# Kernel tuning notes

Measured on AMD Instinct MI355X. Metric: run time of the kernel, lower is better.

Reference implementation:

```python
import jax, jax.numpy as jnp
import numpy as np

B, S, D = 2, 1024, 2048      # batch, seq_len, hidden
H, HD = 16, 128              # heads, head_dim
FF = 8192                    # SwiGLU intermediate
R = 3                        # num_recursion
NEG = -1e9                   # additive mask fill (finfo.min analogue)
TEMP, ALPHA = 1.0, 1.0


def _rmsnorm(x, w, eps=1e-6):
    return x * jax.lax.rsqrt(jnp.mean(x * x, axis=-1, keepdims=True) + eps) * w


def _rot_half(x):
    x1, x2 = jnp.split(x, 2, axis=-1)
    return jnp.concatenate([-x2, x1], axis=-1)


def _block(x, cos, sin, sel, ln1, ln2, Wq, Wk, Wv, Wo, Wg, Wu, Wd):
    # Llama decoder layer restricted to selected tokens.
    # The torch code gathers selected tokens + their rows/cols of the 4D causal
    # mask + their RoPE embeddings, runs dense attention on the packed subset,
    # then scatters back. That is mathematically identical to dense attention
    # over the full sequence where keys are masked to selected tokens and only
    # selected-query outputs are kept (RoPE uses ORIGINAL positions in both).
    b, s, d = x.shape
    h = _rmsnorm(x, ln1)
    q = (h @ Wq).reshape(b, s, H, HD)
    k = (h @ Wk).reshape(b, s, H, HD)
    v = (h @ Wv).reshape(b, s, H, HD)
    cs = cos[None, :, None, :]
    sn = sin[None, :, None, :]
    q = q * cs + _rot_half(q) * sn
    k = k * cs + _rot_half(k) * sn
    scores = jnp.einsum('bqhd,bkhd->bhqk', q, k) / np.float32(np.sqrt(HD))
    causal = jnp.tril(jnp.ones((s, s), dtype=bool))
    allowed = causal[None, None, :, :] & sel[:, None, None, :]  # key must be selected
    attn = jax.nn.softmax(jnp.where(allowed, scores, NEG), axis=-1)
    o = jnp.einsum('bhqk,bkhd->bqhd', attn, v).reshape(b, s, d) @ Wo
    x = x + o
    h2 = _rmsnorm(x, ln2)
    return x + (jax.nn.silu(h2 @ Wg) * (h2 @ Wu)) @ Wd


def setup_inputs() -> dict:
    key = jax.random.key(0)
    ks = jax.random.split(key, 9)
    x = jax.random.normal(ks[0], (B, S, D), dtype=jnp.float32)
    # RoPE tables at original positions (what position_embeddings carries)
    inv_freq = 1.0 / (10000.0 ** (np.arange(0, HD, 2, dtype=np.float32) / HD))
    freqs = np.outer(np.arange(S, dtype=np.float32), inv_freq)
    emb = np.concatenate([freqs, freqs], axis=-1)
    cos = jnp.asarray(np.cos(emb), dtype=jnp.float32)
    sin = jnp.asarray(np.sin(emb), dtype=jnp.float32)
    sc = 0.02
    p = lambda k, shp: jax.random.normal(k, shp, dtype=jnp.float32) * sc
    return dict(
        x=x, cos=cos, sin=sin,
        w_router=p(ks[1], (D, R)),
        ln1=jnp.ones((D,), dtype=jnp.float32),
        ln2=jnp.ones((D,), dtype=jnp.float32),
        Wq=p(ks[2], (D, D)), Wk=p(ks[3], (D, D)),
        Wv=p(ks[4], (D, D)), Wo=p(ks[5], (D, D)),
        Wg=p(ks[6], (D, FF)), Wu=p(ks[7], (D, FF)), Wd=p(ks[8], (FF, D)),
    )


def reference(x, cos, sin, w_router, ln1, ln2, Wq, Wk, Wv, Wo, Wg, Wu, Wd):
    # token-level MoR routing: top-1 depth per token, token at depth r is
    # processed by blocks 0..r and its (weighted) output at depth r is final.
    probs = jax.nn.softmax((x / TEMP) @ w_router, axis=-1) * ALPHA  # [B,S,R]
    top_idx = jnp.argmax(probs, axis=-1)                            # [B,S]
    w = jnp.take_along_axis(probs, top_idx[..., None], axis=-1)     # [B,S,1]
    final_x = x
    cur = x
    for index in range(R):
        sel = top_idx >= index                                      # tokens still active
        out = _block(cur, cos, sin, sel, ln1, ln2, Wq, Wk, Wv, Wo, Wg, Wu, Wd)
        fin = (top_idx == index)[..., None]
        final_x = jnp.where(fin, out * w, final_x)                  # finished: scatter weighted
        cur = jnp.where(sel[..., None], out, cur)                   # continuing: update state
    return final_x
```

## Files before the change

### kernel.cpp

```cpp
#include <hip/hip_runtime.h>
#include <hip/hip_bf16.h>

#define B_  2
#define S_  1024
#define D_  2048
#define H_  16
#define HD_ 128
#define FF_ 8192
#define R_  3
#define T_  (B_*S_)

typedef __attribute__((ext_vector_type(8))) short bf16x8;
typedef __attribute__((ext_vector_type(4))) float f32x4;
using bf16 = __hip_bfloat16;

__device__ __forceinline__ float bf2f(short s) {
    return __uint_as_float(((unsigned)(unsigned short)s) << 16);
}
__device__ __forceinline__ unsigned f2bf_bits(float f) {
    bf16 h = __float2bfloat16(f);
    unsigned short u; __builtin_memcpy(&u, &h, 2);
    return (unsigned)u;
}
__device__ __forceinline__ unsigned pack2(float a, float b) {
    return f2bf_bits(a) | (f2bf_bits(b) << 16);
}
__device__ __forceinline__ float wsum(float v) {
    #pragma unroll
    for (int m = 32; m; m >>= 1) v += __shfl_xor(v, m);
    return v;
}
__device__ __forceinline__ void load_lds16(const void* g, void* l) {
    __builtin_amdgcn_global_load_lds((const __attribute__((address_space(1))) void*)g,
                                     (__attribute__((address_space(3))) void*)l, 16, 0, 0);
}

__global__ __launch_bounds__(256)
void transpose_cast(const float* __restrict__ W, bf16* __restrict__ Wt, int K, int N) {
    __shared__ float tile[32][33];
    const int n0 = blockIdx.x * 32, k0 = blockIdx.y * 32;
    const int c = threadIdx.x & 31, r8 = threadIdx.x >> 5;
    #pragma unroll
    for (int i = 0; i < 4; i++) {
        int r = r8 + i * 8;
        tile[r][c] = W[(long)(k0 + r) * N + n0 + c];
    }
    __syncthreads();
    #pragma unroll
    for (int i = 0; i < 4; i++) {
        int r = r8 + i * 8;
        Wt[(long)(n0 + r) * K + k0 + c] = __float2bfloat16(tile[c][r]);
    }
}

__global__ __launch_bounds__(256)
void router_k(const float* __restrict__ X, const float* __restrict__ Wr,
              int* __restrict__ top, float* __restrict__ wsel) {
    const int t = blockIdx.x * 4 + (threadIdx.x >> 6);
    const int lane = threadIdx.x & 63;
    const float* x = X + (long)t * D_;
    float a0 = 0.f, a1 = 0.f, a2 = 0.f;
    for (int j = lane; j < D_; j += 64) {
        float xv = x[j];
        a0 += xv * Wr[j * 3 + 0];
        a1 += xv * Wr[j * 3 + 1];
        a2 += xv * Wr[j * 3 + 2];
    }
    a0 = wsum(a0); a1 = wsum(a1); a2 = wsum(a2);
    if (lane == 0) {
        int arg = 0; float bm = a0;
        if (a1 > bm) { bm = a1; arg = 1; }
        if (a2 > bm) { bm = a2; arg = 2; }
        float s = expf(a0 - bm) + expf(a1 - bm) + expf(a2 - bm);
        top[t]  = arg;
        wsel[t] = 1.0f / s;
    }
}

__global__ __launch_bounds__(256)
void rmsnorm_k(const float* __restrict__ X, const float* __restrict__ G, bf16* __restrict__ Hb) {
    const int t = blockIdx.x, tid = threadIdx.x;
    const float4* xr = (const float4*)(X + (long)t * D_);
    float4 v0 = xr[tid], v1 = xr[tid + 256];
    float ss = v0.x*v0.x + v0.y*v0.y + v0.z*v0.z + v0.w*v0.w
             + v1.x*v1.x + v1.y*v1.y + v1.z*v1.z + v1.w*v1.w;
    ss = wsum(ss);
    __shared__ float red[4];
    if ((tid & 63) == 0) red[tid >> 6] = ss;
    __syncthreads();
    const float r = rsqrtf((red[0] + red[1] + red[2] + red[3]) * (1.0f / D_) + 1e-6f);
    const float4* gr = (const float4*)G;
    float4 g0 = gr[tid], g1 = gr[tid + 256];
    uint2* ob = (uint2*)(Hb + (long)t * D_);
    uint2 o;
    o.x = pack2(v0.x * r * g0.x, v0.y * r * g0.y);
    o.y = pack2(v0.z * r * g0.z, v0.w * r * g0.w);
    ob[tid] = o;
    o.x = pack2(v1.x * r * g1.x, v1.y * r * g1.y);
    o.y = pack2(v1.z * r * g1.z, v1.w * r * g1.w);
    ob[tid + 256] = o;
}

__global__ __launch_bounds__(256)
void rope_k(bf16* __restrict__ q, bf16* __restrict__ k,
            const float* __restrict__ cosb, const float* __restrict__ sinb) {
    const int idx = blockIdx.x * 256 + threadIdx.x;
    const int d = idx & 63;
    const int h = (idx >> 6) & (H_ - 1);
    const int t = idx >> 10;
    const int s = t & (S_ - 1);
    const long base = (long)t * D_ + h * HD_;
    const float c1 = cosb[s * HD_ + d],      s1 = sinb[s * HD_ + d];
    const float c2 = cosb[s * HD_ + d + 64], s2 = sinb[s * HD_ + d + 64];
    float q1 = __bfloat162float(q[base + d]), q2 = __bfloat162float(q[base + d + 64]);
    q[base + d]      = __float2bfloat16(q1 * c1 - q2 * s1);
    q[base + d + 64] = __float2bfloat16(q2 * c2 + q1 * s2);
    float k1 = __bfloat162float(k[base + d]), k2 = __bfloat162float(k[base + d + 64]);
    k[base + d]      = __float2bfloat16(k1 * c1 - k2 * s1);
    k[base + d + 64] = __float2bfloat16(k2 * c2 + k1 * s2);
}

__global__ __launch_bounds__(256)
void attn_k(const bf16* __restrict__ qb, const bf16* __restrict__ kb, const bf16* __restrict__ vb,
            const int* __restrict__ top, int rec, bf16* __restrict__ aob) {
    __shared__ bf16 Ks[64 * 128];
    __shared__ unsigned Vt[128 * 32];
    __shared__ unsigned short Pt[4][64 * 16];
    const int tid = threadIdx.x, w = tid >> 6, lane = tid & 63;
    const int l15 = lane & 15, lg = lane >> 4;
    const int q0 = blockIdx.x * 64;
    const int h = blockIdx.y, b = blockIdx.z;
    const int qw = q0 + w * 16;

    bf16x8 Qf[4];
    {
        const bf16* qptr = qb + ((long)((b * S_ + qw + l15) * H_ + h)) * HD_ + lg * 8;
        #pragma unroll
        for (int ds = 0; ds < 4; ds++) Qf[ds] = *(const bf16x8*)(qptr + ds * 32);
    }

    f32x4 oacc[8] = {};
    float mrow[4] = {-1e30f, -1e30f, -1e30f, -1e30f};
    float lrow[4] = {0.f, 0.f, 0.f, 0.f};
    const float rs = 0.088388347648318447f;
    const int bsrc = (l15 >> 2) << 4;
    const int jj = l15 & 3;

    const int nch = blockIdx.x + 1;
    for (int kc = 0; kc < nch; kc++) {
        __syncthreads();
        #pragma unroll
        for (int i = 0; i < 4; i++) {
            int r = w * 16 + i * 4 + lg;
            int key = kc * 64 + r;
            const bf16* src = kb + ((long)((b * S_ + key) * H_ + h)) * HD_ + ((l15 ^ (r & 7)) * 8);
            load_lds16(src, &Ks[(w * 16 + i * 4) * 128]);
        }
        #pragma unroll
        for (int i = 0; i < 2; i++) {
            int j = i * 256 + tid;
            int c = j & 15, r2 = (j >> 4) & 31;
            long gv = ((long)((b * S_ + kc * 64 + 2 * r2) * H_ + h)) * HD_ + c * 8;
            uint4 va = *(const uint4*)&vb[gv];
            uint4 vbn = *(const uint4*)&vb[gv + D_];
            const unsigned short* pa = (const unsigned short*)&va;
            const unsigned short* pb = (const unsigned short*)&vbn;
            #pragma unroll
            for (int e = 0; e < 8; e++) {
                int d = c * 8 + e;
                int sw = (d ^ (d >> 3)) & 7;
                Vt[d * 32 + (((r2 >> 2) ^ sw) << 2) + (r2 & 3)] =
                    (unsigned)pa[e] | ((unsigned)pb[e] << 16);
            }
        }
        __syncthreads();

        f32x4 sacc[4] = {};
        #pragma unroll
        for (int kg = 0; kg < 4; kg++) {
            const int row = kg * 16 + l15;
            #pragma unroll
            for (int ds = 0; ds < 4; ds++) {
                bf16x8 kf = *(const bf16x8*)&Ks[row * 128 + (((ds * 4 + lg) ^ (row & 7)) * 8)];
                sacc[kg] = __builtin_amdgcn_mfma_f32_16x16x32_bf16(Qf[ds], kf, sacc[kg], 0, 0, 0);
            }
        }

        int selm[4];
        #pragma unroll
        for (int kg = 0; kg < 4; kg++) {
            int key = kc * 64 + kg * 16 + l15;
            selm[kg] = (top[b * S_ + key] >= rec) ? (key) : (1 << 30);
        }
        float pmat[4][4];
        #pragma unroll
        for (int kg = 0; kg < 4; kg++) {
            #pragma unroll
            for (int j = 0; j < 4; j++) {
                float s = sacc[kg][j] * rs;
                pmat[kg][j] = (selm[kg] <= qw + lg * 4 + j) ? s : -1e9f;
            }
        }
        float scj[4];
        #pragma unroll
        for (int j = 0; j < 4; j++) {
            float tm = fmaxf(fmaxf(pmat[0][j], pmat[1][j]), fmaxf(pmat[2][j], pmat[3][j]));
            #pragma unroll
            for (int m = 1; m < 16; m <<= 1) tm = fmaxf(tm, __shfl_xor(tm, m));
            float mnew = fmaxf(mrow[j], tm);
            scj[j] = __expf(mrow[j] - mnew);
            mrow[j] = mnew;
            float ps = 0.f;
            #pragma unroll
            for (int kg = 0; kg < 4; kg++) {
                float p = __expf(pmat[kg][j] - mnew);
                pmat[kg][j] = p;
                ps += p;
            }
            #pragma unroll
            for (int m = 1; m < 16; m <<= 1) ps += __shfl_xor(ps, m);
            lrow[j] = lrow[j] * scj[j] + ps;
        }
        #pragma unroll
        for (int kg = 0; kg < 4; kg++) {
            uint2 u;
            u.x = pack2(pmat[kg][0], pmat[kg][1]);
            u.y = pack2(pmat[kg][2], pmat[kg][3]);
            *(uint2*)&Pt[w][(kg * 16 + l15) * 16 + lg * 4] = u;
        }
        {
            float t0 = __shfl(scj[0], bsrc), t1 = __shfl(scj[1], bsrc);
            float t2 = __shfl(scj[2], bsrc), t3 = __shfl(scj[3], bsrc);
            float scq = (jj == 0) ? t0 : (jj == 1) ? t1 : (jj == 2) ? t2 : t3;
            #pragma unroll
            for (int dg = 0; dg < 8; dg++) {
                oacc[dg][0] *= scq; oacc[dg][1] *= scq;
                oacc[dg][2] *= scq; oacc[dg][3] *= scq;
            }
        }
        #pragma unroll
        for (int ks = 0; ks < 2; ks++) {
            bf16x8 pf;
            #pragma unroll
            for (int e = 0; e < 8; e++)
                pf[e] = (short)Pt[w][(ks * 32 + lg * 8 + e) * 16 + l15];
            #pragma unroll
            for (int dg = 0; dg < 8; dg++) {
                int d = dg * 16 + l15;
                int sw = (d ^ (d >> 3)) & 7;
                bf16x8 vf = *(const bf16x8*)&Vt[d * 32 + (((ks * 4 + lg) ^ sw) << 2)];
                oacc[dg] = __builtin_amdgcn_mfma_f32_16x16x32_bf16(vf, pf, oacc[dg], 0, 0, 0);
            }
        }
    }
    float u0 = __shfl(lrow[0], bsrc), u1 = __shfl(lrow[1], bsrc);
    float u2 = __shfl(lrow[2], bsrc), u3 = __shfl(lrow[3], bsrc);
    float lq = (jj == 0) ? u0 : (jj == 1) ? u1 : (jj == 2) ? u2 : u3;
    float li = 1.0f / lq;
    const long obase = ((long)((b * S_ + qw + l15) * H_ + h)) * HD_ + lg * 4;
    #pragma unroll
    for (int dg = 0; dg < 8; dg++) {
        #pragma unroll
        for (int jp = 0; jp < 2; jp++) {
            unsigned o = pack2(oacc[dg][jp * 2] * li, oacc[dg][jp * 2 + 1] * li);
            *(unsigned*)&aob[obase + dg * 16 + jp * 2] = o;
        }
    }
}

template<int EP>
__global__ __launch_bounds__(256)
void gemm_k(const bf16* __restrict__ A,
            const bf16* __restrict__ Bt0, const bf16* __restrict__ Bt1, const bf16* __restrict__ Bt2,
            bf16* __restrict__ C0, bf16* __restrict__ C1, bf16* __restrict__ C2,
            const float* __restrict__ resid, float* __restrict__ xout,
            int N, int K) {
    __shared__ bf16 As[128 * 32];
    __shared__ bf16 Bs[128 * 32];
    const int tid = threadIdx.x;
    const int w = tid >> 6, lane = tid & 63;

    const int gx = gridDim.x;
    const int nwg = gx * gridDim.y;
    const int orig = blockIdx.y * gx + blockIdx.x;
    const int qc = nwg >> 3, rc = nwg & 7;
    const int xcd = orig & 7, loc = orig >> 3;
    const int wg = (xcd < rc ? xcd * (qc + 1) : rc * (qc + 1) + (xcd - rc) * qc) + loc;
    const int m0 = (wg % gx) * 128, n0 = (wg / gx) * 128;

    const bf16* Bt = (blockIdx.z == 0) ? Bt0 : ((blockIdx.z == 1) ? Bt1 : Bt2);
    bf16* Cb       = (blockIdx.z == 0) ? C0  : ((blockIdx.z == 1) ? C1  : C2);

    const int srow = lane >> 2;
    const int scol = (lane & 3) * 8;
    const long gA = (long)(m0 + w * 32 + srow) * K + scol;
    const long gB = (long)(n0 + w * 32 + srow) * K + scol;

    const int wr = w >> 1, wc = w & 1;
    const int fm = lane & 15, kg = lane >> 4;

    f32x4 acc[4][4] = {};

    for (int kt = 0; kt < K; kt += 32) {
        __syncthreads();
        #pragma unroll
        for (int i = 0; i < 2; i++) {
            load_lds16(A  + gA + (long)(16 * i) * K + kt, &As[(w * 32 + 16 * i) * 32]);
            load_lds16(Bt + gB + (long)(16 * i) * K + kt, &Bs[(w * 32 + 16 * i) * 32]);
        }
        __syncthreads();
        bf16x8 af[4], bfr[4];
        #pragma unroll
        for (int mi = 0; mi < 4; mi++)
            af[mi] = *(const bf16x8*)&As[(wr * 64 + mi * 16 + fm) * 32 + kg * 8];
        #pragma unroll
        for (int ni = 0; ni < 4; ni++)
            bfr[ni] = *(const bf16x8*)&Bs[(wc * 64 + ni * 16 + fm) * 32 + kg * 8];
        #pragma unroll
        for (int mi = 0; mi < 4; mi++)
            #pragma unroll
            for (int ni = 0; ni < 4; ni++)
                acc[mi][ni] = __builtin_amdgcn_mfma_f32_16x16x32_bf16(af[mi], bfr[ni], acc[mi][ni], 0, 0, 0);
    }
    #pragma unroll
    for (int mi = 0; mi < 4; mi++) {
        #pragma unroll
        for (int j = 0; j < 4; j++) {
            const int m = m0 + wr * 64 + mi * 16 + kg * 4 + j;
            #pragma unroll
            for (int ni = 0; ni < 4; ni++) {
                const int n = n0 + wc * 64 + ni * 16 + fm;
                const long off = (long)m * N + n;
                float v = acc[mi][ni][j];
                if (EP == 0) Cb[off] = __float2bfloat16(v);
                else         xout[off] = v + resid[off];
            }
        }
    }
}

template<int EP>
__global__ __launch_bounds__(512, 2)
void gemm256(const bf16* __restrict__ A, int lda,
             const bf16* __restrict__ Bt0, const bf16* __restrict__ Bt1, int ldb,
             int N, int kz,
             bf16* __restrict__ C0, bf16* __restrict__ C1,
             float* __restrict__ psum) {
    __shared__ bf16 As[2][256 * 64];
    __shared__ bf16 Bs[2][256 * 64];
    const int tid = threadIdx.x;
    const int w = tid >> 6, lane = tid & 63;
    const int z = blockIdx.z;

    const int gx = gridDim.x;
    const int nwg = gx * gridDim.y;
    const int orig = blockIdx.y * gx + blockIdx.x;
    const int qc = nwg >> 3, rc = nwg & 7;
    const int xcd = orig & 7, loc = orig >> 3;
    const int wg = (xcd < rc ? xcd * (qc + 1) : rc * (qc + 1) + (xcd - rc) * qc) + loc;
    const int m0 = (wg % gx) * 256, n0 = (wg / gx) * 256;

    const bf16* Bt = (EP == 0) ? (z ? Bt1 : Bt0) : Bt0;
    const int kBase = (EP == 1) ? z * kz : 0;

    const int wr = w >> 2, wc = w & 3;
    const int fm = lane & 15, kg = lane >> 4;
    const int wchunk = tid & ~63;

    f32x4 acc[8][4] = {};

    auto stage = [&](int buf, int kt) {
        #pragma unroll
        for (int i = 0; i < 4; i++) {
            int c = i * 512 + tid;
            int row = c >> 3, col = (c & 7) * 8;
            load_lds16(A  + (long)(m0 + row) * lda + kBase + kt + col,
                       &As[buf][(i * 512 + wchunk) * 8]);
            load_lds16(Bt + (long)(n0 + row) * ldb + kBase + kt + col,
                       &Bs[buf][(i * 512 + wchunk) * 8]);
        }
    };

    const int nt = kz >> 6;
    stage(0, 0);
    __syncthreads();
    for (int t = 0; t < nt; t++) {
        const int cur = t & 1;
        if (t + 1 < nt) stage(cur ^ 1, (t + 1) << 6);
        #pragma unroll
        for (int kk = 0; kk < 2; kk++) {
            bf16x8 af[8], bfr[4];
            #pragma unroll
            for (int mi = 0; mi < 8; mi++)
                af[mi] = *(const bf16x8*)&As[cur][(wr * 128 + mi * 16 + fm) * 64 + kk * 32 + kg * 8];
            #pragma unroll
            for (int ni = 0; ni < 4; ni++)
                bfr[ni] = *(const bf16x8*)&Bs[cur][(wc * 64 + ni * 16 + fm) * 64 + kk * 32 + kg * 8];
            __builtin_amdgcn_s_setprio(1);
            #pragma unroll
            for (int mi = 0; mi < 8; mi++)
                #pragma unroll
                for (int ni = 0; ni < 4; ni++)
                    acc[mi][ni] = __builtin_amdgcn_mfma_f32_16x16x32_bf16(af[mi], bfr[ni], acc[mi][ni], 0, 0, 0);
            __builtin_amdgcn_s_setprio(0);
        }
        __syncthreads();
    }
    #pragma unroll
    for (int mi = 0; mi < 8; mi++) {
        #pragma unroll
        for (int j = 0; j < 4; j++) {
            const int m = m0 + wr * 128 + mi * 16 + kg * 4 + j;
            #pragma unroll
            for (int ni = 0; ni < 4; ni++) {
                const int n = n0 + wc * 64 + ni * 16 + fm;
                const long off = (long)m * N + n;
                float v = acc[mi][ni][j];
                if (EP == 0) (z ? C1 : C0)[off] = __float2bfloat16(v);
                else         unsafeAtomicAdd(&psum[off], v);
            }
        }
    }
}

__global__ __launch_bounds__(256)
void swiglu_k(const bf16* __restrict__ g, bf16* __restrict__ u) {
    const long i = ((long)blockIdx.x * 256 + threadIdx.x) * 8;
    bf16x8 gv = *(const bf16x8*)&g[i];
    bf16x8 uv = *(const bf16x8*)&u[i];
    uint4 o;
    unsigned* op = (unsigned*)&o;
    #pragma unroll
    for (int p = 0; p < 4; p++) {
        float g0 = bf2f(gv[p * 2]),     u0 = bf2f(uv[p * 2]);
        float g1 = bf2f(gv[p * 2 + 1]), u1 = bf2f(uv[p * 2 + 1]);
        op[p] = pack2(u0 * g0 / (1.f + __expf(-g0)), u1 * g1 / (1.f + __expf(-g1)));
    }
    *(uint4*)&u[i] = o;
}

__global__ __launch_bounds__(256)
void zero_k(float4* __restrict__ p) {
    p[(long)blockIdx.x * 256 + threadIdx.x] = make_float4(0.f, 0.f, 0.f, 0.f);
}

__global__ __launch_bounds__(256)
void reduce_ep3(const float* __restrict__ psum, const float* __restrict__ resid,
                const int* __restrict__ top, const float* __restrict__ wsel,
                float* __restrict__ finalp, float* __restrict__ curp, int rec) {
    const long i = ((long)blockIdx.x * 256 + threadIdx.x) * 4;
    const int m = (int)(i >> 11);
    float4 ps = *(const float4*)&psum[i];
    float4 rs = *(const float4*)&resid[i];
    float4 o = make_float4(ps.x + rs.x, ps.y + rs.y, ps.z + rs.z, ps.w + rs.w);
    const int ti = top[m];
    if (ti == rec) {
        const float wv = wsel[m];
        *(float4*)&finalp[i] = make_float4(o.x * wv, o.y * wv, o.z * wv, o.w * wv);
    }
    if (ti >= rec) *(float4*)&curp[i] = o;
}

extern "C" void kernel_launch(void* const* d_in, const int* in_sizes, int n_in,
                              void* d_out, int out_size, void* d_ws, size_t ws_size,
                              hipStream_t stream) {
    const float* x    = (const float*)d_in[0];
    const float* cosb = (const float*)d_in[1];
    const float* sinb = (const float*)d_in[2];
    const float* wrt  = (const float*)d_in[3];
    const float* ln1  = (const float*)d_in[4];
    const float* ln2  = (const float*)d_in[5];
    const float* Wq   = (const float*)d_in[6];
    const float* Wk   = (const float*)d_in[7];
    const float* Wv   = (const float*)d_in[8];
    const float* Wo   = (const float*)d_in[9];
    const float* Wg   = (const float*)d_in[10];
    const float* Wu   = (const float*)d_in[11];
    const float* Wd   = (const float*)d_in[12];

    char* p = (char*)d_ws;
    auto take = [&](size_t bytes) -> char* {
        char* r = p; p += (bytes + 255) & ~(size_t)255; return r;
    };
    bf16* WqT = (bf16*)take((size_t)D_ * D_ * 2);
    bf16* WkT = (bf16*)take((size_t)D_ * D_ * 2);
    bf16* WvT = (bf16*)take((size_t)D_ * D_ * 2);
    bf16* WoT = (bf16*)take((size_t)D_ * D_ * 2);
    bf16* WgT = (bf16*)take((size_t)D_ * FF_ * 2);
    bf16* WuT = (bf16*)take((size_t)D_ * FF_ * 2);
    bf16* WdT = (bf16*)take((size_t)D_ * FF_ * 2);
    float* cur  = (float*)take((size_t)T_ * D_ * 4);
    float* xnew = (float*)take((size_t)T_ * D_ * 4);
    bf16*  hb   = (bf16*)take((size_t)T_ * D_ * 2);
    bf16*  qb   = (bf16*)take((size_t)T_ * D_ * 2);
    bf16*  kbuf = (bf16*)take((size_t)T_ * D_ * 2);
    bf16*  vbuf = (bf16*)take((size_t)T_ * D_ * 2);
    bf16*  aob  = (bf16*)take((size_t)T_ * D_ * 2);
    bf16*  ub   = (bf16*)take((size_t)T_ * FF_ * 2);
    float* psum = (float*)take((size_t)T_ * D_ * 4);
    int*   top  = (int*)take((size_t)T_ * 4);
    float* wsel = (float*)take((size_t)T_ * 4);
    bf16*  gb   = qb;
    (void)ws_size; (void)in_sizes; (void)n_in; (void)out_size;

    transpose_cast<<<dim3(D_ / 32, D_ / 32), 256, 0, stream>>>(Wq, WqT, D_, D_);
    transpose_cast<<<dim3(D_ / 32, D_ / 32), 256, 0, stream>>>(Wk, WkT, D_, D_);
    transpose_cast<<<dim3(D_ / 32, D_ / 32), 256, 0, stream>>>(Wv, WvT, D_, D_);
    transpose_cast<<<dim3(D_ / 32, D_ / 32), 256, 0, stream>>>(Wo, WoT, D_, D_);
    transpose_cast<<<dim3(FF_ / 32, D_ / 32), 256, 0, stream>>>(Wg, WgT, D_, FF_);
    transpose_cast<<<dim3(FF_ / 32, D_ / 32), 256, 0, stream>>>(Wu, WuT, D_, FF_);
    transpose_cast<<<dim3(D_ / 32, FF_ / 32), 256, 0, stream>>>(Wd, WdT, FF_, D_);

    router_k<<<T_ / 4, 256, 0, stream>>>(x, wrt, top, wsel);

    const float* cur_in = x;
    for (int rec = 0; rec < R_; rec++) {
        rmsnorm_k<<<T_, 256, 0, stream>>>(cur_in, ln1, hb);
        gemm_k<0><<<dim3(T_ / 128, D_ / 128, 3), 256, 0, stream>>>(
            hb, WqT, WkT, WvT, qb, kbuf, vbuf, nullptr, nullptr, D_, D_);
        rope_k<<<(T_ * H_ * 64) / 256, 256, 0, stream>>>(qb, kbuf, cosb, sinb);
        attn_k<<<dim3(S_ / 64, H_, B_), 256, 0, stream>>>(qb, kbuf, vbuf, top, rec, aob);
        gemm_k<1><<<dim3(T_ / 128, D_ / 128, 1), 256, 0, stream>>>(
            aob, WoT, nullptr, nullptr, nullptr, nullptr, nullptr, cur_in, xnew, D_, D_);
        rmsnorm_k<<<T_, 256, 0, stream>>>(xnew, ln2, hb);
        gemm256<0><<<dim3(T_ / 256, FF_ / 256, 2), 512, 0, stream>>>(
            hb, D_, WuT, WgT, D_, FF_, D_, ub, gb, nullptr);
        swiglu_k<<<(T_ * FF_) / (256 * 8), 256, 0, stream>>>(gb, ub);
        zero_k<<<(T_ * D_) / (256 * 4), 256, 0, stream>>>((float4*)psum);
        gemm256<1><<<dim3(T_ / 256, D_ / 256, 4), 512, 0, stream>>>(
            ub, FF_, WdT, nullptr, FF_, D_, D_, nullptr, nullptr, psum);
        reduce_ep3<<<(T_ * D_) / (256 * 4), 256, 0, stream>>>(
            psum, xnew, top, wsel, (float*)d_out, cur, rec);
        cur_in = cur;
    }
}
```

Measured before the change: 1.959 ms.

## Restructure 256x256 GEMM into half-tile staged pipeline with swizzled LDS

Replaces the simple double-buffered k-tile loop in gemm256 with a finer-grained pipeline that stages A/B in 32-wide k halves, keeping several global-to-LDS loads in flight using explicit vmcnt waits and raw s_barrier instead of __syncthreads. The LDS layout packs two rows per 64-element line with an XOR swizzle to reduce bank conflicts on fragment reads. MFMA work is split into two phases per half-tile so LDS reads and new loads interleave with compute. This adds fragile hand-managed waitcnt accounting, which risks races if the counts are wrong.

```diff
diff --git a/kernel.cpp b/kernel.cpp
--- a/kernel.cpp
+++ b/kernel.cpp
@@ -346,8 +346,8 @@
              int N, int kz,
              bf16* __restrict__ C0, bf16* __restrict__ C1,
              float* __restrict__ psum) {
-    __shared__ bf16 As[2][256 * 64];
-    __shared__ bf16 Bs[2][256 * 64];
+    __shared__ bf16 As[32768];
+    __shared__ bf16 Bs[32768];
     const int tid = threadIdx.x;
     const int w = tid >> 6, lane = tid & 63;
     const int z = blockIdx.z;
@@ -365,47 +365,88 @@
 
     const int wr = w >> 2, wc = w & 3;
     const int fm = lane & 15, kg = lane >> 4;
-    const int wchunk = tid & ~63;
+    const int nt = kz >> 6;
 
     f32x4 acc[8][4] = {};
 
-    auto stage = [&](int buf, int kt) {
-        #pragma unroll
-        for (int i = 0; i < 4; i++) {
-            int c = i * 512 + tid;
-            int row = c >> 3, col = (c & 7) * 8;
-            load_lds16(A  + (long)(m0 + row) * lda + kBase + kt + col,
-                       &As[buf][(i * 512 + wchunk) * 8]);
-            load_lds16(Bt + (long)(n0 + row) * ldb + kBase + kt + col,
-                       &Bs[buf][(i * 512 + wchunk) * 8]);
+    auto stage_half = [&](int h) {
+        if (h >= 4 * nt) return;
+        const int th = h >> 2, khh = (h >> 1) & 1, isB = h & 1, bufh = th & 1;
+        bf16* dst = (isB ? Bs : As) + (bufh * 2 + khh) * 8192;
+        const bf16* srcm = isB ? Bt : A;
+        const long ldx = isB ? (long)ldb : (long)lda;
+        const int rb = isB ? n0 : m0;
+        const long colb = (long)kBase + th * 64 + khh * 32;
+        #pragma unroll
+        for (int j = 0; j < 2; ++j) {
+            const int L = j * 64 + (w << 3) + (lane >> 3);
+            const int cl = (lane & 7) ^ (L & 7);
+            const bf16* g = srcm + (long)(rb + 2 * L + (cl >> 2)) * ldx + colb + (cl & 3) * 8;
+            load_lds16(g, dst + (j * 64 + (w << 3)) * 64);
         }
     };
 
-    const int nt = kz >> 6;
-    stage(0, 0);
-    __syncthreads();
-    for (int t = 0; t < nt; t++) {
-        const int cur = t & 1;
-        if (t + 1 < nt) stage(cur ^ 1, (t + 1) << 6);
-        #pragma unroll
-        for (int kk = 0; kk < 2; kk++) {
-            bf16x8 af[8], bfr[4];
-            #pragma unroll
-            for (int mi = 0; mi < 8; mi++)
-                af[mi] = *(const bf16x8*)&As[cur][(wr * 128 + mi * 16 + fm) * 64 + kk * 32 + kg * 8];
-            #pragma unroll
-            for (int ni = 0; ni < 4; ni++)
-                bfr[ni] = *(const bf16x8*)&Bs[cur][(wc * 64 + ni * 16 + fm) * 64 + kk * 32 + kg * 8];
-            __builtin_amdgcn_s_setprio(1);
-            #pragma unroll
-            for (int mi = 0; mi < 8; mi++)
-                #pragma unroll
-                for (int ni = 0; ni < 4; ni++)
-                    acc[mi][ni] = __builtin_amdgcn_mfma_f32_16x16x32_bf16(af[mi], bfr[ni], acc[mi][ni], 0, 0, 0);
-            __builtin_amdgcn_s_setprio(0);
-        }
-        __syncthreads();
-    }
+    stage_half(0); stage_half(1); stage_half(2); stage_half(3); stage_half(4);
+    asm volatile("s_waitcnt vmcnt(6)" ::: "memory");
+    __builtin_amdgcn_s_barrier();
+
+    for (int g0 = 0; g0 < 4 * nt; g0 += 2) {
+        const int t = g0 >> 2, kh = (g0 >> 1) & 1, buf = t & 1;
+        const bf16* ra  = As + (buf * 2 + kh) * 8192;
+        const bf16* rbb = Bs + (buf * 2 + kh) * 8192;
+        bf16x8 af[8], b01[2];
+        #pragma unroll
+        for (int mi = 0; mi < 8; ++mi) {
+            const int row = wr * 128 + mi * 16 + fm;
+            const int L = row >> 1;
+            const int cp = ((row & 1) * 4 + kg) ^ (L & 7);
+            af[mi] = *(const bf16x8*)(ra + L * 64 + cp * 8);
+        }
+        #pragma unroll
+        for (int ni = 0; ni < 2; ++ni) {
+            const int row = wc * 64 + ni * 16 + fm;
+            const int L = row >> 1;
+            const int cp = ((row & 1) * 4 + kg) ^ (L & 7);
+            b01[ni] = *(const bf16x8*)(rbb + L * 64 + cp * 8);
+        }
+        stage_half(g0 + 5);
+        __builtin_amdgcn_s_barrier();
+        asm volatile("s_waitcnt lgkmcnt(0)" ::: "memory");
+        __builtin_amdgcn_sched_barrier(0);
+        __builtin_amdgcn_s_setprio(1);
+        #pragma unroll
+        for (int mi = 0; mi < 8; ++mi) {
+            acc[mi][0] = __builtin_amdgcn_mfma_f32_16x16x32_bf16(af[mi], b01[0], acc[mi][0], 0, 0, 0);
+            acc[mi][1] = __builtin_amdgcn_mfma_f32_16x16x32_bf16(af[mi], b01[1], acc[mi][1], 0, 0, 0);
+        }
+        __builtin_amdgcn_s_setprio(0);
+        __builtin_amdgcn_s_barrier();
+        bf16x8 b23[2];
+        #pragma unroll
+        for (int ni = 0; ni < 2; ++ni) {
+            const int row = wc * 64 + (ni + 2) * 16 + fm;
+            const int L = row >> 1;
+            const int cp = ((row & 1) * 4 + kg) ^ (L & 7);
+            b23[ni] = *(const bf16x8*)(rbb + L * 64 + cp * 8);
+        }
+        stage_half(g0 + 6);
+        __builtin_amdgcn_s_barrier();
+        asm volatile("s_waitcnt lgkmcnt(0)" ::: "memory");
+        __builtin_amdgcn_sched_barrier(0);
+        __builtin_amdgcn_s_setprio(1);
+        #pragma unroll
+        for (int mi = 0; mi < 8; ++mi) {
+            acc[mi][2] = __builtin_amdgcn_mfma_f32_16x16x32_bf16(af[mi], b23[0], acc[mi][2], 0, 0, 0);
+            acc[mi][3] = __builtin_amdgcn_mfma_f32_16x16x32_bf16(af[mi], b23[1], acc[mi][3], 0, 0, 0);
+        }
+        __builtin_amdgcn_s_setprio(0);
+        const int remp = 4 * nt - g0;
+        if (remp >= 8)      asm volatile("s_waitcnt vmcnt(6)" ::: "memory");
+        else if (remp == 6) asm volatile("s_waitcnt vmcnt(4)" ::: "memory");
+        else if (remp == 4) asm volatile("s_waitcnt vmcnt(0)" ::: "memory");
+        __builtin_amdgcn_s_barrier();
+    }
+
     #pragma unroll
     for (int mi = 0; mi < 8; mi++) {
         #pragma unroll
```

Result: faster. 1.839 ms (-6.1%).
